# Kernel tuning notes

Hardware: AMD Instinct MI355X
Metric: run time of the kernel (lower is better)

The kernel has to match this reference:

```python
import jax, jax.numpy as jnp
import numpy as np


def setup_inputs() -> dict:
    key = jax.random.key(0)
    k1, k2 = jax.random.split(key)
    B, IN, OUT = 1024, 512, 256
    m = jax.random.uniform(k1, (B, IN), dtype=jnp.float32)       # fuzzy memberships in [0,1]
    weight = jax.random.normal(k2, (IN, OUT), dtype=jnp.float32)  # raw weights, clamped in forward
    return {"m": m, "weight": weight}


def reference(m, weight):
    # wf = clamp(weight, 0, 1)
    w = jnp.clip(weight, 0.0, 1.0)
    # min_max: out[b, o] = max_i min(m[b, i], w[i, o])  (tropical-style matmul)
    # broadcast [B, IN, 1] vs [1, IN, OUT] -> min -> max over IN
    inter = jnp.minimum(m[:, :, None], w[None, :, :])  # [B, IN, OUT]
    return jnp.max(inter, axis=1)                       # [B, OUT]
```

## Files before the change

kernel.cpp:

```cpp
#include <hip/hip_runtime.h>
#include <cstdint>


constexpr int IN  = 512;
constexpr int OUT = 256;

static __device__ __forceinline__ float clamp01(float x) {
  return fminf(fmaxf(x, 0.0f), 1.0f);
}

__global__ __launch_bounds__(256, 4)
void minmax_topk(const float* __restrict__ m, const float* __restrict__ w,
                 float* __restrict__ out) {
  __shared__ int   cnt[32];
  __shared__ int   start[32];
  __shared__ int   ord[IN];
  __shared__ float mv[IN];
  __shared__ int   flags[IN / 8];

  const int tid = threadIdx.x;
  const int b   = blockIdx.x;
  const float* mrow = m + (size_t)b * IN;

  if (tid < 32) cnt[tid] = 0;
  if (tid < IN / 8) flags[tid] = 1;
  __syncthreads();

  const float v0 = mrow[tid];
  const float v1 = mrow[tid + 256];
  const int q0 = min((int)(v0 * 32.0f), 31);
  const int q1 = min((int)(v1 * 32.0f), 31);
  atomicAdd(&cnt[q0], 1);
  atomicAdd(&cnt[q1], 1);
  __syncthreads();

  if (tid == 0) {
    int off = 0;
    for (int q = 31; q >= 0; --q) { start[q] = off; off += cnt[q]; }
  }
  __syncthreads();

  {
    int p0 = atomicAdd(&start[q0], 1); ord[p0] = tid;       mv[p0] = v0;
    int p1 = atomicAdd(&start[q1], 1); ord[p1] = tid + 256; mv[p1] = v1;
  }
  __syncthreads();

  float acc = 0.0f;
  int p = 0;
  while (true) {
    const float m0 = mv[p + 0]; const int i0 = ord[p + 0];
    const float m1 = mv[p + 1]; const int i1 = ord[p + 1];
    const float m2 = mv[p + 2]; const int i2 = ord[p + 2];
    const float m3 = mv[p + 3]; const int i3 = ord[p + 3];
    const float m4 = mv[p + 4]; const int i4 = ord[p + 4];
    const float m5 = mv[p + 5]; const int i5 = ord[p + 5];
    const float m6 = mv[p + 6]; const int i6 = ord[p + 6];
    const float m7 = mv[p + 7]; const int i7 = ord[p + 7];
    const float w0 = w[(size_t)i0 * OUT + tid];
    const float w1 = w[(size_t)i1 * OUT + tid];
    const float w2 = w[(size_t)i2 * OUT + tid];
    const float w3 = w[(size_t)i3 * OUT + tid];
    const float w4 = w[(size_t)i4 * OUT + tid];
    const float w5 = w[(size_t)i5 * OUT + tid];
    const float w6 = w[(size_t)i6 * OUT + tid];
    const float w7 = w[(size_t)i7 * OUT + tid];
    acc = fmaxf(acc, fminf(m0, clamp01(w0)));
    acc = fmaxf(acc, fminf(m1, clamp01(w1)));
    acc = fmaxf(acc, fminf(m2, clamp01(w2)));
    acc = fmaxf(acc, fminf(m3, clamp01(w3)));
    acc = fmaxf(acc, fminf(m4, clamp01(w4)));
    acc = fmaxf(acc, fminf(m5, clamp01(w5)));
    acc = fmaxf(acc, fminf(m6, clamp01(w6)));
    acc = fmaxf(acc, fminf(m7, clamp01(w7)));

    p += 8;
    if (p >= IN) break;

    const int   qn    = min((int)(mv[p] * 32.0f), 31);
    const float bound = (float)(qn + 1) * 0.03125f;
    const int   slot  = (p >> 3) - 1;
    if (acc < bound) flags[slot] = 0;
    __syncthreads();
    const int done = flags[slot];
    if (done) break;
  }

  out[(size_t)b * OUT + tid] = acc;
}

extern "C" void kernel_launch(void* const* d_in, const int* in_sizes, int n_in,
                              void* d_out, int out_size, void* d_ws, size_t ws_size,
                              hipStream_t stream) {
  (void)n_in; (void)out_size; (void)d_ws; (void)ws_size;
  const float* m = (const float*)d_in[0];
  const float* w = (const float*)d_in[1];
  float* out = (float*)d_out;
  const int B = in_sizes[0] / IN;
  minmax_topk<<<dim3(B), 256, 0, stream>>>(m, w, out);
}
```

Baseline: 60.99 us.

## Use warp-scan offsets, barrier-AND early exit, and unconditional first chunks

Replaces the single-thread serial bucket prefix sum with a 32-lane shuffle scan. Swaps the shared-memory flag array plus barrier for a block-wide __syncthreads_and vote as the early-exit test. Processes the first 32 sorted inputs before any exit check, so the first few per-chunk barriers are skipped. The cost is extra work whenever the bound would already have been met within those first 32 inputs.

```diff
diff --git a/kernel.cpp b/kernel.cpp
--- a/kernel.cpp
+++ b/kernel.cpp
@@ -16,14 +16,12 @@
   __shared__ int   start[32];
   __shared__ int   ord[IN];
   __shared__ float mv[IN];
-  __shared__ int   flags[IN / 8];
 
   const int tid = threadIdx.x;
   const int b   = blockIdx.x;
   const float* mrow = m + (size_t)b * IN;
 
   if (tid < 32) cnt[tid] = 0;
-  if (tid < IN / 8) flags[tid] = 1;
   __syncthreads();
 
   const float v0 = mrow[tid];
@@ -34,9 +32,16 @@
   atomicAdd(&cnt[q1], 1);
   __syncthreads();
 
-  if (tid == 0) {
-    int off = 0;
-    for (int q = 31; q >= 0; --q) { start[q] = off; off += cnt[q]; }
+  if (tid < 32) {
+    const int q = 31 - tid;
+    const int x = cnt[q];
+    int incl = x;
+#pragma unroll
+    for (int o = 1; o < 32; o <<= 1) {
+      int t = __shfl_up(incl, o, 32);
+      if (tid >= o) incl += t;
+    }
+    start[q] = incl - x;
   }
   __syncthreads();
 
@@ -47,44 +52,47 @@
   __syncthreads();
 
   float acc = 0.0f;
-  int p = 0;
-  while (true) {
-    const float m0 = mv[p + 0]; const int i0 = ord[p + 0];
-    const float m1 = mv[p + 1]; const int i1 = ord[p + 1];
-    const float m2 = mv[p + 2]; const int i2 = ord[p + 2];
-    const float m3 = mv[p + 3]; const int i3 = ord[p + 3];
-    const float m4 = mv[p + 4]; const int i4 = ord[p + 4];
-    const float m5 = mv[p + 5]; const int i5 = ord[p + 5];
-    const float m6 = mv[p + 6]; const int i6 = ord[p + 6];
-    const float m7 = mv[p + 7]; const int i7 = ord[p + 7];
-    const float w0 = w[(size_t)i0 * OUT + tid];
-    const float w1 = w[(size_t)i1 * OUT + tid];
-    const float w2 = w[(size_t)i2 * OUT + tid];
-    const float w3 = w[(size_t)i3 * OUT + tid];
-    const float w4 = w[(size_t)i4 * OUT + tid];
-    const float w5 = w[(size_t)i5 * OUT + tid];
-    const float w6 = w[(size_t)i6 * OUT + tid];
-    const float w7 = w[(size_t)i7 * OUT + tid];
-    acc = fmaxf(acc, fminf(m0, clamp01(w0)));
-    acc = fmaxf(acc, fminf(m1, clamp01(w1)));
-    acc = fmaxf(acc, fminf(m2, clamp01(w2)));
-    acc = fmaxf(acc, fminf(m3, clamp01(w3)));
-    acc = fmaxf(acc, fminf(m4, clamp01(w4)));
-    acc = fmaxf(acc, fminf(m5, clamp01(w5)));
-    acc = fmaxf(acc, fminf(m6, clamp01(w6)));
-    acc = fmaxf(acc, fminf(m7, clamp01(w7)));
 
-    p += 8;
-    if (p >= IN) break;
+#define CHUNK8(P)                                                         \
+  {                                                                       \
+    const float cm0 = mv[(P) + 0]; const int ci0 = ord[(P) + 0];          \
+    const float cm1 = mv[(P) + 1]; const int ci1 = ord[(P) + 1];          \
+    const float cm2 = mv[(P) + 2]; const int ci2 = ord[(P) + 2];          \
+    const float cm3 = mv[(P) + 3]; const int ci3 = ord[(P) + 3];          \
+    const float cm4 = mv[(P) + 4]; const int ci4 = ord[(P) + 4];          \
+    const float cm5 = mv[(P) + 5]; const int ci5 = ord[(P) + 5];          \
+    const float cm6 = mv[(P) + 6]; const int ci6 = ord[(P) + 6];          \
+    const float cm7 = mv[(P) + 7]; const int ci7 = ord[(P) + 7];          \
+    const float cw0 = w[(size_t)ci0 * OUT + tid];                         \
+    const float cw1 = w[(size_t)ci1 * OUT + tid];                         \
+    const float cw2 = w[(size_t)ci2 * OUT + tid];                         \
+    const float cw3 = w[(size_t)ci3 * OUT + tid];                         \
+    const float cw4 = w[(size_t)ci4 * OUT + tid];                         \
+    const float cw5 = w[(size_t)ci5 * OUT + tid];                         \
+    const float cw6 = w[(size_t)ci6 * OUT + tid];                         \
+    const float cw7 = w[(size_t)ci7 * OUT + tid];                         \
+    acc = fmaxf(acc, fminf(cm0, clamp01(cw0)));                           \
+    acc = fmaxf(acc, fminf(cm1, clamp01(cw1)));                           \
+    acc = fmaxf(acc, fminf(cm2, clamp01(cw2)));                           \
+    acc = fmaxf(acc, fminf(cm3, clamp01(cw3)));                           \
+    acc = fmaxf(acc, fminf(cm4, clamp01(cw4)));                           \
+    acc = fmaxf(acc, fminf(cm5, clamp01(cw5)));                           \
+    acc = fmaxf(acc, fminf(cm6, clamp01(cw6)));                           \
+    acc = fmaxf(acc, fminf(cm7, clamp01(cw7)));                           \
+  }
 
+  CHUNK8(0)
+  CHUNK8(8)
+  CHUNK8(16)
+  CHUNK8(24)
+
+  for (int p = 32; p < IN; p += 8) {
     const int   qn    = min((int)(mv[p] * 32.0f), 31);
     const float bound = (float)(qn + 1) * 0.03125f;
-    const int   slot  = (p >> 3) - 1;
-    if (acc < bound) flags[slot] = 0;
-    __syncthreads();
-    const int done = flags[slot];
-    if (done) break;
+    if (__syncthreads_and(acc >= bound)) break;
+    CHUNK8(p)
   }
+#undef CHUNK8
 
   out[(size_t)b * OUT + tid] = acc;
 }
```

Result: slower. 62.51 us (+2.5%).
